# Kernel tuning notes

Hardware: AMD Instinct MI355X
Metric: run time of the kernel (lower is better)

Reference implementation:

```python
import jax, jax.numpy as jnp
import numpy as np

B, N = 32, 512
NFEAT, NHID, NCLASS, NHEADS = 128, 64, 128, 8
WORK_D, SUB_D = 32, 32
H1, H2, OUT_D = 256, 256, 512
ALPHA = 0.2
NEG = -9e15


def setup_inputs() -> dict:
    key = jax.random.key(0)
    ks = jax.random.split(key, 16)
    return {
        "graph_inf": jax.random.normal(ks[0], (B, N, NFEAT), jnp.float32),
        "graph_matrix": jax.random.randint(ks[1], (B, N, N), 0, 2, jnp.int32),
        "masks": jnp.ones((B, N), jnp.float32),
        "node_order": jax.random.randint(ks[2], (B,), 0, N, jnp.int64),
        "work": jax.random.normal(ks[3], (B, WORK_D), jnp.float32),
        "subtask": jax.random.normal(ks[4], (B, SUB_D), jnp.float32),
        # GAT head params
        "W_heads": jax.random.normal(ks[5], (NHEADS, NFEAT, NHID), jnp.float32) * 0.1,
        "a_heads": jax.random.normal(ks[6], (NHEADS, 2 * NHID), jnp.float32) * 0.1,
        "W_out": jax.random.normal(ks[7], (NHID * NHEADS, NCLASS), jnp.float32) * 0.05,
        "a_out": jax.random.normal(ks[8], (2 * NCLASS,), jnp.float32) * 0.1,
        # MLP encoder params
        "fc1_w": jax.random.normal(ks[9], (NCLASS + WORK_D + SUB_D, H1), jnp.float32) * 0.07,
        "fc1_b": jnp.zeros((H1,), jnp.float32),
        "fc2_w": jax.random.normal(ks[10], (H1, H2), jnp.float32) * 0.06,
        "fc2_b": jnp.zeros((H2,), jnp.float32),
        "fc3_w": jax.random.normal(ks[11], (H2, OUT_D), jnp.float32) * 0.06,
        "fc3_b": jnp.zeros((OUT_D,), jnp.float32),
    }


def _gat_layer(Wh, a1, a2, adj, masks):
    # Wh: [B,N,F]; additive GAT score e_ij = leakyrelu(a1.Wh_i + a2.Wh_j)
    s1 = Wh @ a1  # [B,N]
    s2 = Wh @ a2  # [B,N]
    e = jax.nn.leaky_relu(s1[:, :, None] + s2[:, None, :], ALPHA)  # [B,N,N]
    att = jax.nn.softmax(jnp.where(adj > 0, e, NEG), axis=2)
    h_prime = jnp.einsum('bnm,bmf->bnf', att, Wh)
    return h_prime * masks[:, :, None]


def reference(graph_inf, graph_matrix, masks, node_order, work, subtask,
              W_heads, a_heads, W_out, a_out,
              fc1_w, fc1_b, fc2_w, fc2_b, fc3_w, fc3_b):
    adj = graph_matrix
    # multi-head GAT layer (concat=True -> ELU)
    def head(Wk, ak):
        Wh = jnp.einsum('bnf,fo->bno', graph_inf, Wk)
        return jax.nn.elu(_gat_layer(Wh, ak[:NHID], ak[NHID:], adj, masks))
    xh = jax.vmap(head)(W_heads, a_heads)  # [H,B,N,NHID]
    x = jnp.transpose(xh, (1, 2, 0, 3)).reshape(B, N, NHEADS * NHID)
    # output GAT layer (concat=False)
    Wh = jnp.einsum('bnf,fo->bno', x, W_out)
    x = _gat_layer(Wh, a_out[:NCLASS], a_out[NCLASS:], adj, masks)
    x = x * masks[:, :, None]
    # select subtask node per batch element
    selected = x[jnp.arange(B), node_order]  # [B,NCLASS]
    inf = jnp.concatenate([selected, work, subtask], axis=1)
    h = jax.nn.relu(inf @ fc1_w + fc1_b)
    h = jax.nn.relu(h @ fc2_w + fc2_b)
    out = h @ fc3_w + fc3_b
    return jax.nn.softmax(out, axis=-1)
```

## Files before the change

### kernel.cpp

```cpp
#include <hip/hip_runtime.h>

typedef unsigned short u16;
typedef unsigned int u32;
typedef unsigned long long u64;

typedef __bf16 bf16x8 __attribute__((ext_vector_type(8)));
typedef float f32x4 __attribute__((ext_vector_type(4)));

#define LOG2E 1.44269504088896340736f

__device__ __forceinline__ float b2f(u16 u) {
    u32 x = ((u32)u) << 16;
    return __builtin_bit_cast(float, x);
}
__device__ __forceinline__ u16 f2b(float f) {
    u32 u = __builtin_bit_cast(u32, f);
    u32 r = (u + 0x7fffu + ((u >> 16) & 1u)) >> 16;
    return (u16)r;
}
__device__ __forceinline__ float ld(const void* p, int i, bool bf) {
    return bf ? b2f(((const u16*)p)[i]) : ((const float*)p)[i];
}
__device__ __forceinline__ bool detect_bf16(const void* masks) {
    return ((const u16*)masks)[0] != 0;
}
__device__ __forceinline__ f32x4 mfma16(bf16x8 a, bf16x8 b, f32x4 c) {
    return __builtin_amdgcn_mfma_f32_16x16x32_bf16(a, b, c, 0, 0, 0);
}

__device__ __attribute__((aligned(256))) u32  g_adjm[16384 * 16];
__device__ __attribute__((aligned(256))) u16  g_BT1[512 * 128];
__device__ __attribute__((aligned(256))) u16  g_BT2[128 * 512];
__device__ __attribute__((aligned(256))) u16  g_Xc[32 * 512 * 128];
__device__ __attribute__((aligned(256))) u16  g_xb[16384 * 512];
__device__ __attribute__((aligned(256))) u16  g_Wh2[16384 * 128];
__device__ __attribute__((aligned(256))) float g_s1b[16384];
__device__ __attribute__((aligned(256))) float g_s2b[16384];
__device__ __attribute__((aligned(256))) u16  g_fc1T[256 * 192];
__device__ __attribute__((aligned(256))) u16  g_fc2T[256 * 256];
__device__ __attribute__((aligned(256))) u16  g_fc3T[512 * 256];
__device__ __attribute__((aligned(256))) u16  g_Ahi[32 * 192];
__device__ __attribute__((aligned(256))) u16  g_Alo[32 * 192];
__device__ __attribute__((aligned(256))) u16  g_H1hi[32 * 256];
__device__ __attribute__((aligned(256))) u16  g_H1lo[32 * 256];
__device__ __attribute__((aligned(256))) u16  g_H2hi[32 * 256];
__device__ __attribute__((aligned(256))) u16  g_H2lo[32 * 256];
__device__ __attribute__((aligned(256))) float g_logits[32 * 512];

__global__ __launch_bounds__(256) void prep_kernel(
    const int* __restrict__ adj, const void* __restrict__ Whd,
    const void* __restrict__ Wo, const void* __restrict__ Xin,
    const void* __restrict__ fc1w, const void* __restrict__ fc2w,
    const void* __restrict__ fc3w, const void* __restrict__ masks)
{
    const bool bf = detect_bf16(masks);
    const int blk = blockIdx.x;
    const int tid = threadIdx.x;
    if (blk < 1024) {
        int id = blk * 256 + tid;
        int row = id >> 4, w = id & 15;
        const int4* p = (const int4*)(adj + row * 512 + w * 32);
        int4 v[8];
        #pragma unroll
        for (int s = 0; s < 8; ++s) v[s] = p[s];
        u32 word = 0;
        #pragma unroll
        for (int s = 0; s < 8; ++s) {
            u32 nib = (v[s].x > 0 ? 1u : 0u) | (v[s].y > 0 ? 2u : 0u) |
                      (v[s].z > 0 ? 4u : 0u) | (v[s].w > 0 ? 8u : 0u);
            word |= nib << (4 * s);
        }
        g_adjm[id] = word;
    } else if (blk < 1028) {
        int base = (blk - 1024) * 16384;
        for (int e = base + tid; e < base + 16384; e += 256) {
            int n = e >> 7, k = e & 127;
            g_BT1[e] = f2b(ld(Whd, (n >> 6) * 8192 + k * 64 + (n & 63), bf));
        }
    } else if (blk < 1032) {
        int base = (blk - 1028) * 16384;
        for (int e = base + tid; e < base + 16384; e += 256) {
            int n = e >> 9, k = e & 511;
            g_BT2[e] = f2b(ld(Wo, k * 128 + n, bf));
        }
    } else if (blk < 1288) {
        if (!bf) {
            int base = (blk - 1032) * 8192;
            for (int e = base + tid; e < base + 8192; e += 256)
                g_Xc[e] = f2b(((const float*)Xin)[e]);
        }
    } else if (blk < 1294) {
        int base = (blk - 1288) * 8192;
        for (int e = base + tid; e < base + 8192; e += 256) {
            int n = e / 192, k = e - n * 192;
            g_fc1T[e] = f2b(ld(fc1w, k * 256 + n, bf));
        }
    } else if (blk < 1302) {
        int base = (blk - 1294) * 8192;
        for (int e = base + tid; e < base + 8192; e += 256) {
            int n = e >> 8, k = e & 255;
            g_fc2T[e] = f2b(ld(fc2w, k * 256 + n, bf));
        }
    } else {
        int base = (blk - 1302) * 8192;
        for (int e = base + tid; e < base + 8192; e += 256) {
            int n = e >> 8, k = e & 255;
            g_fc3T[e] = f2b(ld(fc3w, k * 512 + n, bf));
        }
    }
}

__global__ __launch_bounds__(1024, 1) void gat1_kernel(
    const void* __restrict__ Xin, const void* __restrict__ a_heads,
    const void* __restrict__ masks)
{
    __shared__ __attribute__((aligned(16))) u16 WhL[64 * 520];
    __shared__ __attribute__((aligned(16))) u16 As[64 * 136];
    __shared__ __attribute__((aligned(16))) u16 XcL[128 * 136];
    __shared__ float s1p[4][512];
    __shared__ float s2p[4][512];
    __shared__ float E2s[512];
    __shared__ float E2ps[512];

    const bool bf = detect_bf16(masks);
    const int tid = threadIdx.x;
    const int w = tid >> 6, lane = tid & 63;
    const int c = lane & 15, q = lane >> 4;
    const int b = blockIdx.x & 31;
    const int h = blockIdx.x >> 5;

    const u16* Bsrc = bf ? (const u16*)Xin : g_Xc;

    {
        int r = tid >> 4, seg = (tid & 15) * 8;
        *(uint4*)&As[r * 136 + seg] = *(const uint4*)(g_BT1 + (h * 64 + r) * 128 + seg);
    }

    const int wm = w & 3, wn = w >> 2;
    float a1v[4], a2v[4];
    #pragma unroll
    for (int i = 0; i < 4; ++i) {
        int o = wm * 16 + q * 4 + i;
        a1v[i] = ld(a_heads, h * 128 + o, bf);
        a2v[i] = ld(a_heads, h * 128 + 64 + o, bf);
    }

    const int pr = tid >> 3, pseg = (tid & 7) * 16;
    uint4 xr0, xr1;
    {
        const u16* src = Bsrc + (b * 512 + pr) * 128 + pseg;
        xr0 = *(const uint4*)src;
        xr1 = *(const uint4*)(src + 8);
    }

    for (int chunk = 0; chunk < 4; ++chunk) {
        __syncthreads();
        *(uint4*)&XcL[pr * 136 + pseg] = xr0;
        *(uint4*)&XcL[pr * 136 + pseg + 8] = xr1;
        if (chunk < 3) {
            const u16* src = Bsrc + (b * 512 + (chunk + 1) * 128 + pr) * 128 + pseg;
            xr0 = *(const uint4*)src;
            xr1 = *(const uint4*)(src + 8);
        }
        __syncthreads();
        f32x4 cacc[2] = {};
        #pragma unroll
        for (int kt = 0; kt < 4; ++kt) {
            bf16x8 af = *(const bf16x8*)&As[(wm * 16 + c) * 136 + kt * 32 + q * 8];
            #pragma unroll
            for (int nt = 0; nt < 2; ++nt) {
                bf16x8 bv = *(const bf16x8*)&XcL[(wn * 32 + nt * 16 + c) * 136 + kt * 32 + q * 8];
                cacc[nt] = mfma16(af, bv, cacc[nt]);
            }
        }
        #pragma unroll
        for (int nt = 0; nt < 2; ++nt) {
            const int ncol = chunk * 128 + wn * 32 + nt * 16 + c;
            float p1 = 0.f, p2 = 0.f;
            #pragma unroll
            for (int i = 0; i < 4; ++i) {
                float v = cacc[nt][i];
                WhL[(wm * 16 + q * 4 + i) * 520 + ncol] = f2b(v);
                p1 += v * a1v[i];
                p2 += v * a2v[i];
            }
            p1 += __shfl_xor(p1, 16); p1 += __shfl_xor(p1, 32);
            p2 += __shfl_xor(p2, 16); p2 += __shfl_xor(p2, 32);
            if (lane < 16) {
                int n = chunk * 128 + wn * 32 + nt * 16 + lane;
                s1p[wm][n] = p1;
// ... 74 lines not shown
        #pragma unroll
        for (int i = 0; i < 4; ++i) {
            float lr = __shfl(acc1[g][i], (lane & 48));
            float invr = (lr == 0.f) ? (1.f / 512.f) : (1.f / lr);
            const int row = R + q * 4 + i;
            float mk = ld(masks, b * 512 + row, bf);
            #pragma unroll
            for (int nt = 0; nt < 4; ++nt) {
                float v = acc[g][nt][i] * invr * mk;
                float o = v > 0.f ? v : (__expf(v) - 1.f);
                g_xb[(b * 512 + row) * 512 + h * 64 + nt * 16 + c] = f2b(o);
            }
        }
    }
}

__global__ __launch_bounds__(256, 2) void gemm2_kernel(
    const void* __restrict__ a_out, const void* __restrict__ masks)
{
    __shared__ __attribute__((aligned(16))) u16 Asl[64 * 72];
    __shared__ __attribute__((aligned(16))) u16 Bsl[128 * 72];
    const int tid = threadIdx.x;
    const int w = tid >> 6, lane = tid & 63;
    const int c = lane & 15, q = lane >> 4;
    const int tm = blockIdx.x * 64;
    const int rowA = tid >> 2, shA = (tid & 3) * 16;
    const int rowB = tid >> 1, shB = (tid & 1) * 32;
    f32x4 acc[8] = {};
    for (int kc = 0; kc < 512; kc += 64) {
        __syncthreads();
        const u16* Ag = g_xb + (tm + rowA) * 512 + kc + shA;
        *(uint4*)&Asl[rowA * 72 + shA] = *(const uint4*)Ag;
        *(uint4*)&Asl[rowA * 72 + shA + 8] = *(const uint4*)(Ag + 8);
        const u16* Bg = g_BT2 + rowB * 512 + kc + shB;
        #pragma unroll
        for (int s = 0; s < 4; ++s)
            *(uint4*)&Bsl[rowB * 72 + shB + 8 * s] = *(const uint4*)(Bg + 8 * s);
        __syncthreads();
        #pragma unroll
        for (int kt = 0; kt < 2; ++kt) {
            bf16x8 av = *(const bf16x8*)&Asl[(w * 16 + c) * 72 + kt * 32 + q * 8];
            #pragma unroll
            for (int ct = 0; ct < 8; ++ct) {
                bf16x8 bv = *(const bf16x8*)&Bsl[(ct * 16 + c) * 72 + kt * 32 + q * 8];
                acc[ct] = mfma16(av, bv, acc[ct]);
            }
        }
    }
    const bool bf = detect_bf16(masks);
    float a1v[8], a2v[8];
    #pragma unroll
    for (int ct = 0; ct < 8; ++ct) {
        a1v[ct] = ld(a_out, ct * 16 + c, bf);
        a2v[ct] = ld(a_out, 128 + ct * 16 + c, bf);
    }
    #pragma unroll
    for (int i = 0; i < 4; ++i) {
        float p1 = 0.f, p2 = 0.f;
        #pragma unroll
        for (int ct = 0; ct < 8; ++ct) {
            p1 += acc[ct][i] * a1v[ct];
            p2 += acc[ct][i] * a2v[ct];
        }
        #pragma unroll
        for (int off = 1; off < 16; off <<= 1) {
            p1 += __shfl_xor(p1, off);
            p2 += __shfl_xor(p2, off);
        }
        if (c == 0) {
            int m = tm + w * 16 + q * 4 + i;
            g_s1b[m] = p1 * LOG2E;
            g_s2b[m] = p2 * LOG2E;
        }
    }
    #pragma unroll
    for (int ct = 0; ct < 8; ++ct)
        #pragma unroll
        for (int i = 0; i < 4; ++i) {
            int m = tm + w * 16 + q * 4 + i;
            g_Wh2[m * 128 + ct * 16 + c] = f2b(acc[ct][i]);
        }
}

__global__ __launch_bounds__(256) void fin_att(
    const void* __restrict__ masks, const int* __restrict__ node_order,
    const void* __restrict__ workv, const void* __restrict__ subtaskv)
{
    __shared__ float att[512];
    __shared__ float parts[16][128];
    __shared__ float redl[4];

    const bool bf = detect_bf16(masks);
    const int b = blockIdx.x, t = threadIdx.x;
    const int lane = t & 63, wv = t >> 6;
    const int istar = node_order[b];

    const float s1v = g_s1b[b * 512 + istar];
    const u32* arow = g_adjm + (b * 512 + istar) * 16;
    float ssum = 0.f;
    #pragma unroll
    for (int rep = 0; rep < 2; ++rep) {
        int j = t + rep * 256;
        float e = s1v + g_s2b[b * 512 + j];
        e = fmaxf(e, 0.2f * e);
        float ex = ((arow[j >> 5] >> (j & 31)) & 1u) ? exp2f(e) : 0.f;
        att[j] = ex;
        ssum += ex;
    }
    for (int off = 1; off < 64; off <<= 1) ssum += __shfl_xor(ssum, off);
    if (lane == 0) redl[wv] = ssum;
    __syncthreads();
    float tot = redl[0] + redl[1] + redl[2] + redl[3];
    bool uni = (tot == 0.f);
    float inv = uni ? (1.f / 512.f) : (1.f / tot);

    const int og = t & 15, jg = t >> 4;
    float acc[8] = {};
    const u16* base = g_Wh2 + (b * 512 + jg * 32) * 128 + og * 8;
    #pragma unroll 8
    for (int j0 = 0; j0 < 32; ++j0) {
        float wgt = uni ? 1.f : att[jg * 32 + j0];
        union { u16 u[8]; uint4 v; } z;
        z.v = *(const uint4*)(base + j0 * 128);
        #pragma unroll
        for (int i = 0; i < 8; ++i) acc[i] += wgt * b2f(z.u[i]);
    }
    #pragma unroll
    for (int i = 0; i < 8; ++i) parts[jg][og * 8 + i] = acc[i];
    __syncthreads();
    float mk = ld(masks, b * 512 + istar, bf);
    if (t < 128) {
        float s = 0.f;
        #pragma unroll
        for (int jj = 0; jj < 16; ++jj) s += parts[jj][t];
        s *= inv * mk * mk;
        u16 hi = f2b(s);
        g_Ahi[b * 192 + t] = hi;
        g_Alo[b * 192 + t] = f2b(s - b2f(hi));
    } else if (t < 160) {
        g_Ahi[b * 192 + t] = bf ? ((const u16*)workv)[b * 32 + t - 128]
                                : f2b(((const float*)workv)[b * 32 + t - 128]);
        g_Alo[b * 192 + t] = 0;
    } else if (t < 192) {
        g_Ahi[b * 192 + t] = bf ? ((const u16*)subtaskv)[b * 32 + t - 160]
                                : f2b(((const float*)subtaskv)[b * 32 + t - 160]);
        g_Alo[b * 192 + t] = 0;
    }
}

template<int K, int NOUT, bool RELU>
__device__ __forceinline__ void mlp_body(
    const u16* __restrict__ Ahi, const u16* __restrict__ Alo,
    const u16* __restrict__ WT, const void* __restrict__ bias,
    u16* __restrict__ Ohi, u16* __restrict__ Olo, float* __restrict__ Of,
    const void* __restrict__ masks)
{
    const bool bf = detect_bf16(masks);
    const int t = threadIdx.x, w = t >> 6, lane = t & 63;
    const int c = lane & 15, q = lane >> 4;
    const int col = blockIdx.x * 64 + w * 16 + c;

    const u16* wp  = WT + col * K + q * 8;
    const u16* ahp = Ahi + c * K + q * 8;
    const u16* alp = Alo + c * K + q * 8;

    f32x4 acc0 = {}, acc1 = {};
    #pragma unroll
    for (int kt = 0; kt < K / 32; ++kt) {
        bf16x8 bw  = *(const bf16x8*)(wp + kt * 32);
        bf16x8 ah0 = *(const bf16x8*)(ahp + kt * 32);
        bf16x8 al0 = *(const bf16x8*)(alp + kt * 32);
        bf16x8 ah1 = *(const bf16x8*)(ahp + 16 * K + kt * 32);
        bf16x8 al1 = *(const bf16x8*)(alp + 16 * K + kt * 32);
        acc0 = mfma16(ah0, bw, acc0);
        acc0 = mfma16(al0, bw, acc0);
        acc1 = mfma16(ah1, bw, acc1);
        acc1 = mfma16(al1, bw, acc1);
    }
    float bs = ld(bias, col, bf);
    #pragma unroll
    for (int mt = 0; mt < 2; ++mt) {
        f32x4 a = mt ? acc1 : acc0;
        #pragma unroll
        for (int i = 0; i < 4; ++i) {
            int m = mt * 16 + q * 4 + i;
            float v = a[i] + bs;
            if (RELU) {
                v = fmaxf(v, 0.f);
                u16 hi = f2b(v);
                Ohi[m * NOUT + col] = hi;
                Olo[m * NOUT + col] = f2b(v - b2f(hi));
            } else {
                Of[m * NOUT + col] = v;
            }
        }
    }
}

__global__ __launch_bounds__(256) void mlp1_kernel(const void* bias, const void* masks) {
    mlp_body<192, 256, true>(g_Ahi, g_Alo, g_fc1T, bias, g_H1hi, g_H1lo, nullptr, masks);
}
__global__ __launch_bounds__(256) void mlp2_kernel(const void* bias, const void* masks) {
    mlp_body<256, 256, true>(g_H1hi, g_H1lo, g_fc2T, bias, g_H2hi, g_H2lo, nullptr, masks);
}
__global__ __launch_bounds__(256) void mlp3_kernel(const void* bias, const void* masks) {
    mlp_body<256, 512, false>(g_H2hi, g_H2lo, g_fc3T, bias, nullptr, nullptr, g_logits, masks);
}

__global__ __launch_bounds__(64) void softmax_kernel(
    const void* __restrict__ masks, void* __restrict__ out)
{
    const bool bf = detect_bf16(masks);
    const int row = blockIdx.x, lane = threadIdx.x;
    const float* lp = g_logits + row * 512 + lane * 8;
    float v[8];
    *(float4*)&v[0] = *(const float4*)lp;
    *(float4*)&v[4] = *(const float4*)(lp + 4);
    float mx = v[0];
    #pragma unroll
    for (int i = 1; i < 8; ++i) mx = fmaxf(mx, v[i]);
    for (int off = 1; off < 64; off <<= 1) mx = fmaxf(mx, __shfl_xor(mx, off));
    float e[8];
    float s = 0.f;
    #pragma unroll
    for (int i = 0; i < 8; ++i) { e[i] = __expf(v[i] - mx); s += e[i]; }
    for (int off = 1; off < 64; off <<= 1) s += __shfl_xor(s, off);
    float inv = 1.f / s;
    if (bf) {
        u16* o = (u16*)out + row * 512 + lane * 8;
        #pragma unroll
        for (int i = 0; i < 8; ++i) o[i] = f2b(e[i] * inv);
    } else {
        float* o = (float*)out + row * 512 + lane * 8;
        #pragma unroll
        for (int i = 0; i < 8; ++i) o[i] = e[i] * inv;
    }
}

extern "C" void kernel_launch(void* const* d_in, const int* in_sizes, int n_in,
                              void* d_out, int out_size, void* d_ws, size_t ws_size,
                              hipStream_t stream)
{
    const void* graph_inf    = d_in[0];
    const int*  graph_matrix = (const int*)d_in[1];
    const void* masks        = d_in[2];
    const int*  node_order   = (const int*)d_in[3];
    const void* work         = d_in[4];
    const void* subtask      = d_in[5];
    const void* W_heads      = d_in[6];
    const void* a_heads      = d_in[7];
    const void* W_out        = d_in[8];
    const void* a_out        = d_in[9];
    const void* fc1w         = d_in[10];
    const void* fc1b         = d_in[11];
    const void* fc2w         = d_in[12];
    const void* fc2b         = d_in[13];
    const void* fc3w         = d_in[14];
    const void* fc3b         = d_in[15];

    prep_kernel<<<dim3(1318), dim3(256), 0, stream>>>(graph_matrix, W_heads, W_out, graph_inf,
                                                      fc1w, fc2w, fc3w, masks);
    gat1_kernel<<<dim3(256), dim3(1024), 0, stream>>>(graph_inf, a_heads, masks);
    gemm2_kernel<<<dim3(256), dim3(256), 0, stream>>>(a_out, masks);
    fin_att<<<dim3(32), dim3(256), 0, stream>>>(masks, node_order, work, subtask);
    mlp1_kernel<<<dim3(4), dim3(256), 0, stream>>>(fc1b, masks);
    mlp2_kernel<<<dim3(4), dim3(256), 0, stream>>>(fc2b, masks);
    mlp3_kernel<<<dim3(8), dim3(256), 0, stream>>>(fc3b, masks);
    softmax_kernel<<<dim3(32), dim3(64), 0, stream>>>(masks, d_out);
}
```

Baseline: 184.8 us.

## Fuse attention readout, MLP and softmax into a single tail kernel

Replaces the final attention row kernel, three MFMA MLP kernels and the softmax kernel with one per-batch kernel that keeps the intermediate activations in shared memory and uses scalar FMAs. The MLP weights are read directly from the inputs, so the transposes in the prep kernel are removed. This cuts four launches and the global round trips between stages. In exchange, each of the 32 blocks streams all MLP weights itself, and the matmuls no longer use matrix cores.

```diff
diff --git a/kernel.cpp b/kernel.cpp
--- a/kernel.cpp
+++ b/kernel.cpp
@@ -20,6 +20,10 @@
 }
 __device__ __forceinline__ float ld(const void* p, int i, bool bf) {
     return bf ? b2f(((const u16*)p)[i]) : ((const float*)p)[i];
+}
+template<bool BF>
+__device__ __forceinline__ float ldt(const void* p, int i) {
+    return BF ? b2f(((const u16*)p)[i]) : ((const float*)p)[i];
 }
 __device__ __forceinline__ bool detect_bf16(const void* masks) {
     return ((const u16*)masks)[0] != 0;
@@ -36,22 +40,11 @@
 __device__ __attribute__((aligned(256))) u16  g_Wh2[16384 * 128];
 __device__ __attribute__((aligned(256))) float g_s1b[16384];
 __device__ __attribute__((aligned(256))) float g_s2b[16384];
-__device__ __attribute__((aligned(256))) u16  g_fc1T[256 * 192];
-__device__ __attribute__((aligned(256))) u16  g_fc2T[256 * 256];
-__device__ __attribute__((aligned(256))) u16  g_fc3T[512 * 256];
-__device__ __attribute__((aligned(256))) u16  g_Ahi[32 * 192];
-__device__ __attribute__((aligned(256))) u16  g_Alo[32 * 192];
-__device__ __attribute__((aligned(256))) u16  g_H1hi[32 * 256];
-__device__ __attribute__((aligned(256))) u16  g_H1lo[32 * 256];
-__device__ __attribute__((aligned(256))) u16  g_H2hi[32 * 256];
-__device__ __attribute__((aligned(256))) u16  g_H2lo[32 * 256];
-__device__ __attribute__((aligned(256))) float g_logits[32 * 512];
 
 __global__ __launch_bounds__(256) void prep_kernel(
     const int* __restrict__ adj, const void* __restrict__ Whd,
     const void* __restrict__ Wo, const void* __restrict__ Xin,
-    const void* __restrict__ fc1w, const void* __restrict__ fc2w,
-    const void* __restrict__ fc3w, const void* __restrict__ masks)
+    const void* __restrict__ masks)
 {
     const bool bf = detect_bf16(masks);
     const int blk = blockIdx.x;
@@ -83,29 +76,11 @@
             int n = e >> 9, k = e & 511;
             g_BT2[e] = f2b(ld(Wo, k * 128 + n, bf));
         }
-    } else if (blk < 1288) {
+    } else {
         if (!bf) {
             int base = (blk - 1032) * 8192;
             for (int e = base + tid; e < base + 8192; e += 256)
                 g_Xc[e] = f2b(((const float*)Xin)[e]);
-        }
-    } else if (blk < 1294) {
-        int base = (blk - 1288) * 8192;
-        for (int e = base + tid; e < base + 8192; e += 256) {
-            int n = e / 192, k = e - n * 192;
-            g_fc1T[e] = f2b(ld(fc1w, k * 256 + n, bf));
-        }
-    } else if (blk < 1302) {
-        int base = (blk - 1294) * 8192;
-        for (int e = base + tid; e < base + 8192; e += 256) {
-            int n = e >> 8, k = e & 255;
-            g_fc2T[e] = f2b(ld(fc2w, k * 256 + n, bf));
-        }
-    } else {
-        int base = (blk - 1302) * 8192;
-        for (int e = base + tid; e < base + 8192; e += 256) {
-            int n = e >> 8, k = e & 255;
-            g_fc3T[e] = f2b(ld(fc3w, k * 512 + n, bf));
         }
     }
 }
@@ -346,15 +321,17 @@
         }
 }
 
-__global__ __launch_bounds__(256) void fin_att(
+template<bool BF>
+__device__ __forceinline__ void tail_body(
     const void* __restrict__ masks, const int* __restrict__ node_order,
-    const void* __restrict__ workv, const void* __restrict__ subtaskv)
+    const void* __restrict__ workv, const void* __restrict__ subtaskv,
+    const void* __restrict__ fc1w, const void* __restrict__ fc1b,
+    const void* __restrict__ fc2w, const void* __restrict__ fc2b,
+    const void* __restrict__ fc3w, const void* __restrict__ fc3b,
+    void* __restrict__ out,
+    float* att, float (*parts)[128], float* redl, float* red2,
+    float* inf_s, float* h1s, float* h2s)
 {
-    __shared__ float att[512];
-    __shared__ float parts[16][128];
-    __shared__ float redl[4];
-
-    const bool bf = detect_bf16(masks);
     const int b = blockIdx.x, t = threadIdx.x;
     const int lane = t & 63, wv = t >> 6;
     const int istar = node_order[b];
@@ -392,113 +369,108 @@
     #pragma unroll
     for (int i = 0; i < 8; ++i) parts[jg][og * 8 + i] = acc[i];
     __syncthreads();
-    float mk = ld(masks, b * 512 + istar, bf);
+
+    float mk = ldt<BF>(masks, b * 512 + istar);
     if (t < 128) {
         float s = 0.f;
         #pragma unroll
         for (int jj = 0; jj < 16; ++jj) s += parts[jj][t];
-        s *= inv * mk * mk;
-        u16 hi = f2b(s);
-        g_Ahi[b * 192 + t] = hi;
-        g_Alo[b * 192 + t] = f2b(s - b2f(hi));
+        inf_s[t] = s * inv * mk * mk;
     } else if (t < 160) {
-        g_Ahi[b * 192 + t] = bf ? ((const u16*)workv)[b * 32 + t - 128]
-                                : f2b(((const float*)workv)[b * 32 + t - 128]);
-        g_Alo[b * 192 + t] = 0;
+        inf_s[t] = ldt<BF>(workv, b * 32 + t - 128);
     } else if (t < 192) {
-        g_Ahi[b * 192 + t] = bf ? ((const u16*)subtaskv)[b * 32 + t - 160]
-                                : f2b(((const float*)subtaskv)[b * 32 + t - 160]);
-        g_Alo[b * 192 + t] = 0;
-    }
-}
-
-template<int K, int NOUT, bool RELU>
-__device__ __forceinline__ void mlp_body(
-    const u16* __restrict__ Ahi, const u16* __restrict__ Alo,
-    const u16* __restrict__ WT, const void* __restrict__ bias,
-    u16* __restrict__ Ohi, u16* __restrict__ Olo, float* __restrict__ Of,
-    const void* __restrict__ masks)
+        inf_s[t] = ldt<BF>(subtaskv, b * 32 + t - 160);
+    }
+    __syncthreads();
+
+    {
+        float a0 = 0.f, a1 = 0.f, a2 = 0.f, a3 = 0.f;
+        #pragma unroll 4
+        for (int k = 0; k < 192; k += 4) {
+            a0 += inf_s[k]     * ldt<BF>(fc1w, k * 256 + t);
+            a1 += inf_s[k + 1] * ldt<BF>(fc1w, (k + 1) * 256 + t);
+            a2 += inf_s[k + 2] * ldt<BF>(fc1w, (k + 2) * 256 + t);
+            a3 += inf_s[k + 3] * ldt<BF>(fc1w, (k + 3) * 256 + t);
+        }
+        float v = (a0 + a1) + (a2 + a3) + ldt<BF>(fc1b, t);
+        h1s[t] = fmaxf(v, 0.f);
+    }
+    __syncthreads();
+
+    {
+        float a0 = 0.f, a1 = 0.f, a2 = 0.f, a3 = 0.f;
+        #pragma unroll 4
+        for (int k = 0; k < 256; k += 4) {
+            a0 += h1s[k]     * ldt<BF>(fc2w, k * 256 + t);
+            a1 += h1s[k + 1] * ldt<BF>(fc2w, (k + 1) * 256 + t);
+            a2 += h1s[k + 2] * ldt<BF>(fc2w, (k + 2) * 256 + t);
+            a3 += h1s[k + 3] * ldt<BF>(fc2w, (k + 3) * 256 + t);
+        }
+        float v = (a0 + a1) + (a2 + a3) + ldt<BF>(fc2b, t);
+        h2s[t] = fmaxf(v, 0.f);
+    }
+    __syncthreads();
+
+    float lg0, lg1;
+    {
+        float b0 = 0.f, b1 = 0.f, c0 = 0.f, c1 = 0.f;
+        #pragma unroll 4
+        for (int k = 0; k < 256; k += 2) {
+            float hv0 = h2s[k], hv1 = h2s[k + 1];
+            b0 += hv0 * ldt<BF>(fc3w, k * 512 + t);
+            c0 += hv0 * ldt<BF>(fc3w, k * 512 + 256 + t);
+            b1 += hv1 * ldt<BF>(fc3w, (k + 1) * 512 + t);
+            c1 += hv1 * ldt<BF>(fc3w, (k + 1) * 512 + 256 + t);
+        }
+        lg0 = b0 + b1 + ldt<BF>(fc3b, t);
+        lg1 = c0 + c1 + ldt<BF>(fc3b, 256 + t);
+    }
+
+    float mx = fmaxf(lg0, lg1);
+    #pragma unroll
+    for (int off = 1; off < 64; off <<= 1) mx = fmaxf(mx, __shfl_xor(mx, off));
+    if (lane == 0) redl[wv] = mx;
+    __syncthreads();
+    mx = fmaxf(fmaxf(redl[0], redl[1]), fmaxf(redl[2], redl[3]));
+    float e0 = __expf(lg0 - mx), e1 = __expf(lg1 - mx);
+    float s = e0 + e1;
+    #pragma unroll
+    for (int off = 1; off < 64; off <<= 1) s += __shfl_xor(s, off);
+    if (lane == 0) red2[wv] = s;
+    __syncthreads();
+    float invs = 1.f / (red2[0] + red2[1] + red2[2] + red2[3]);
+    if (BF) {
+        u16* o = (u16*)out + b * 512;
+        o[t]       = f2b(e0 * invs);
+        o[256 + t] = f2b(e1 * invs);
+    } else {
+        float* o = (float*)out + b * 512;
+        o[t]       = e0 * invs;
+        o[256 + t] = e1 * invs;
+    }
+}
+
+__global__ __launch_bounds__(256) void tail_kernel(
+    const void* __restrict__ masks, const int* __restrict__ node_order,
+    const void* __restrict__ workv, const void* __restrict__ subtaskv,
+    const void* __restrict__ fc1w, const void* __restrict__ fc1b,
+    const void* __restrict__ fc2w, const void* __restrict__ fc2b,
+    const void* __restrict__ fc3w, const void* __restrict__ fc3b,
+    void* __restrict__ out)
 {
-    const bool bf = detect_bf16(masks);
-    const int t = threadIdx.x, w = t >> 6, lane = t & 63;
-    const int c = lane & 15, q = lane >> 4;
-    const int col = blockIdx.x * 64 + w * 16 + c;
-
-    const u16* wp  = WT + col * K + q * 8;
-    const u16* ahp = Ahi + c * K + q * 8;
-    const u16* alp = Alo + c * K + q * 8;
-
-    f32x4 acc0 = {}, acc1 = {};
-    #pragma unroll
-    for (int kt = 0; kt < K / 32; ++kt) {
-        bf16x8 bw  = *(const bf16x8*)(wp + kt * 32);
-        bf16x8 ah0 = *(const bf16x8*)(ahp + kt * 32);
-        bf16x8 al0 = *(const bf16x8*)(alp + kt * 32);
-        bf16x8 ah1 = *(const bf16x8*)(ahp + 16 * K + kt * 32);
-        bf16x8 al1 = *(const bf16x8*)(alp + 16 * K + kt * 32);
-        acc0 = mfma16(ah0, bw, acc0);
-        acc0 = mfma16(al0, bw, acc0);
-        acc1 = mfma16(ah1, bw, acc1);
-        acc1 = mfma16(al1, bw, acc1);
-    }
-    float bs = ld(bias, col, bf);
-    #pragma unroll
-    for (int mt = 0; mt < 2; ++mt) {
-        f32x4 a = mt ? acc1 : acc0;
-        #pragma unroll
-        for (int i = 0; i < 4; ++i) {
-            int m = mt * 16 + q * 4 + i;
-            float v = a[i] + bs;
-            if (RELU) {
-                v = fmaxf(v, 0.f);
-                u16 hi = f2b(v);
-                Ohi[m * NOUT + col] = hi;
-                Olo[m * NOUT + col] = f2b(v - b2f(hi));
-            } else {
-                Of[m * NOUT + col] = v;
-            }
-        }
-    }
-}
-
-__global__ __launch_bounds__(256) void mlp1_kernel(const void* bias, const void* masks) {
-    mlp_body<192, 256, true>(g_Ahi, g_Alo, g_fc1T, bias, g_H1hi, g_H1lo, nullptr, masks);
-}
-__global__ __launch_bounds__(256) void mlp2_kernel(const void* bias, const void* masks) {
-    mlp_body<256, 256, true>(g_H1hi, g_H1lo, g_fc2T, bias, g_H2hi, g_H2lo, nullptr, masks);
-}
-__global__ __launch_bounds__(256) void mlp3_kernel(const void* bias, const void* masks) {
-    mlp_body<256, 512, false>(g_H2hi, g_H2lo, g_fc3T, bias, nullptr, nullptr, g_logits, masks);
-}
-
-__global__ __launch_bounds__(64) void softmax_kernel(
-    const void* __restrict__ masks, void* __restrict__ out)
-{
-    const bool bf = detect_bf16(masks);
-    const int row = blockIdx.x, lane = threadIdx.x;
-    const float* lp = g_logits + row * 512 + lane * 8;
-    float v[8];
-    *(float4*)&v[0] = *(const float4*)lp;
-    *(float4*)&v[4] = *(const float4*)(lp + 4);
-    float mx = v[0];
-    #pragma unroll
-    for (int i = 1; i < 8; ++i) mx = fmaxf(mx, v[i]);
-    for (int off = 1; off < 64; off <<= 1) mx = fmaxf(mx, __shfl_xor(mx, off));
-    float e[8];
-    float s = 0.f;
-    #pragma unroll
-    for (int i = 0; i < 8; ++i) { e[i] = __expf(v[i] - mx); s += e[i]; }
-    for (int off = 1; off < 64; off <<= 1) s += __shfl_xor(s, off);
-    float inv = 1.f / s;
-    if (bf) {
-        u16* o = (u16*)out + row * 512 + lane * 8;
-        #pragma unroll
-        for (int i = 0; i < 8; ++i) o[i] = f2b(e[i] * inv);
-    } else {
-        float* o = (float*)out + row * 512 + lane * 8;
-        #pragma unroll
-        for (int i = 0; i < 8; ++i) o[i] = e[i] * inv;
-    }
+    __shared__ float att[512];
+    __shared__ float parts[16][128];
+    __shared__ float redl[4];
+    __shared__ float red2[4];
+    __shared__ float inf_s[192];
+    __shared__ float h1s[256];
+    __shared__ float h2s[256];
+    if (detect_bf16(masks))
+        tail_body<true>(masks, node_order, workv, subtaskv, fc1w, fc1b, fc2w, fc2b,
+                        fc3w, fc3b, out, att, parts, redl, red2, inf_s, h1s, h2s);
+    else
+        tail_body<false>(masks, node_order, workv, subtaskv, fc1w, fc1b, fc2w, fc2b,
+                         fc3w, fc3b, out, att, parts, redl, red2, inf_s, h1s, h2s);
 }
 
 extern "C" void kernel_launch(void* const* d_in, const int* in_sizes, int n_in,
@@ -522,13 +494,11 @@
     const void* fc3w         = d_in[14];
     const void* fc3b         = d_in[15];
 
-    prep_kernel<<<dim3(1318), dim3(256), 0, stream>>>(graph_matrix, W_heads, W_out, graph_inf,
-                                                      fc1w, fc2w, fc3w, masks);
+    prep_kernel<<<dim3(1288), dim3(256), 0, stream>>>(graph_matrix, W_heads, W_out,
+                                                      graph_inf, masks);
     gat1_kernel<<<dim3(256), dim3(1024), 0, stream>>>(graph_inf, a_heads, masks);
     gemm2_kernel<<<dim3(256), dim3(256), 0, stream>>>(a_out, masks);
-    fin_att<<<dim3(32), dim3(256), 0, stream>>>(masks, node_order, work, subtask);
-    mlp1_kernel<<<dim3(4), dim3(256), 0, stream>>>(fc1b, masks);
-    mlp2_kernel<<<dim3(4), dim3(256), 0, stream>>>(fc2b, masks);
-    mlp3_kernel<<<dim3(8), dim3(256), 0, stream>>>(fc3b, masks);
-    softmax_kernel<<<dim3(32), dim3(64), 0, stream>>>(masks, d_out);
-}
+    tail_kernel<<<dim3(32), dim3(256), 0, stream>>>(masks, node_order, work, subtask,
+                                                    fc1w, fc1b, fc2w, fc2b, fc3w, fc3b,
+                                                    d_out);
+}
```

Result: slower. 193.0 us (+4.4%).

## Fuse three MLP layers and softmax into one single-block kernel

Applied to the files above, without the earlier changes.

Replaces the four small launches (mlp1, mlp2, mlp3, softmax) with one 1024-thread block that keeps the hidden activations in LDS and does the softmax with cross-wave reductions. This removes three kernel launches and the global round trips for the intermediate activations and logits. The cost is that all MLP work now runs on a single CU instead of several, so the weight loads and MFMAs are serialized on one compute unit.

```diff
diff --git a/kernel.cpp b/kernel.cpp
--- a/kernel.cpp
+++ b/kernel.cpp
@@ -41,11 +41,6 @@
 __device__ __attribute__((aligned(256))) u16  g_fc3T[512 * 256];
 __device__ __attribute__((aligned(256))) u16  g_Ahi[32 * 192];
 __device__ __attribute__((aligned(256))) u16  g_Alo[32 * 192];
-__device__ __attribute__((aligned(256))) u16  g_H1hi[32 * 256];
-__device__ __attribute__((aligned(256))) u16  g_H1lo[32 * 256];
-__device__ __attribute__((aligned(256))) u16  g_H2hi[32 * 256];
-__device__ __attribute__((aligned(256))) u16  g_H2lo[32 * 256];
-__device__ __attribute__((aligned(256))) float g_logits[32 * 512];
 
 __global__ __launch_bounds__(256) void prep_kernel(
     const int* __restrict__ adj, const void* __restrict__ Whd,
@@ -412,93 +407,179 @@
     }
 }
 
-template<int K, int NOUT, bool RELU>
-__device__ __forceinline__ void mlp_body(
-    const u16* __restrict__ Ahi, const u16* __restrict__ Alo,
-    const u16* __restrict__ WT, const void* __restrict__ bias,
-    u16* __restrict__ Ohi, u16* __restrict__ Olo, float* __restrict__ Of,
-    const void* __restrict__ masks)
+__global__ __launch_bounds__(1024) void mlp_fused(
+    const void* __restrict__ fc1b, const void* __restrict__ fc2b,
+    const void* __restrict__ fc3b, const void* __restrict__ masks,
+    void* __restrict__ out)
 {
+    __shared__ __attribute__((aligned(16))) u16 H1hi[32 * 264];
+    __shared__ __attribute__((aligned(16))) u16 H1lo[32 * 264];
+    __shared__ __attribute__((aligned(16))) u16 H2hi[32 * 264];
+    __shared__ __attribute__((aligned(16))) u16 H2lo[32 * 264];
+    __shared__ float pred[32][16];
+    __shared__ float rred[32];
+
     const bool bf = detect_bf16(masks);
     const int t = threadIdx.x, w = t >> 6, lane = t & 63;
     const int c = lane & 15, q = lane >> 4;
-    const int col = blockIdx.x * 64 + w * 16 + c;
-
-    const u16* wp  = WT + col * K + q * 8;
-    const u16* ahp = Ahi + c * K + q * 8;
-    const u16* alp = Alo + c * K + q * 8;
-
-    f32x4 acc0 = {}, acc1 = {};
-    #pragma unroll
-    for (int kt = 0; kt < K / 32; ++kt) {
-        bf16x8 bw  = *(const bf16x8*)(wp + kt * 32);
-        bf16x8 ah0 = *(const bf16x8*)(ahp + kt * 32);
-        bf16x8 al0 = *(const bf16x8*)(alp + kt * 32);
-        bf16x8 ah1 = *(const bf16x8*)(ahp + 16 * K + kt * 32);
-        bf16x8 al1 = *(const bf16x8*)(alp + 16 * K + kt * 32);
-        acc0 = mfma16(ah0, bw, acc0);
-        acc0 = mfma16(al0, bw, acc0);
-        acc1 = mfma16(ah1, bw, acc1);
-        acc1 = mfma16(al1, bw, acc1);
-    }
-    float bs = ld(bias, col, bf);
-    #pragma unroll
-    for (int mt = 0; mt < 2; ++mt) {
-        f32x4 a = mt ? acc1 : acc0;
+
+    {
+        const int col = w * 16 + c;
+        const u16* wp  = g_fc1T + col * 192 + q * 8;
+        const u16* ahp = g_Ahi + c * 192 + q * 8;
+        const u16* alp = g_Alo + c * 192 + q * 8;
+        f32x4 acc0 = {}, acc1 = {};
+        #pragma unroll
+        for (int kt = 0; kt < 6; ++kt) {
+            bf16x8 bw  = *(const bf16x8*)(wp + kt * 32);
+            bf16x8 ah0 = *(const bf16x8*)(ahp + kt * 32);
+            bf16x8 al0 = *(const bf16x8*)(alp + kt * 32);
+            bf16x8 ah1 = *(const bf16x8*)(ahp + 16 * 192 + kt * 32);
+            bf16x8 al1 = *(const bf16x8*)(alp + 16 * 192 + kt * 32);
+            acc0 = mfma16(ah0, bw, acc0);
+            acc0 = mfma16(al0, bw, acc0);
+            acc1 = mfma16(ah1, bw, acc1);
+            acc1 = mfma16(al1, bw, acc1);
+        }
+        float bs = ld(fc1b, col, bf);
+        #pragma unroll
+        for (int mt = 0; mt < 2; ++mt) {
+            f32x4 a = mt ? acc1 : acc0;
+            #pragma unroll
+            for (int i = 0; i < 4; ++i) {
+                int m = mt * 16 + q * 4 + i;
+                float v = fmaxf(a[i] + bs, 0.f);
+                u16 hi = f2b(v);
+                H1hi[m * 264 + col] = hi;
+                H1lo[m * 264 + col] = f2b(v - b2f(hi));
+            }
+        }
+    }
+    __syncthreads();
+
+    {
+        const int col = w * 16 + c;
+        const u16* wp  = g_fc2T + col * 256 + q * 8;
+        const u16* ahp = H1hi + c * 264 + q * 8;
+        const u16* alp = H1lo + c * 264 + q * 8;
+        f32x4 acc0 = {}, acc1 = {};
+        #pragma unroll
+        for (int kt = 0; kt < 8; ++kt) {
+            bf16x8 bw  = *(const bf16x8*)(wp + kt * 32);
+            bf16x8 ah0 = *(const bf16x8*)(ahp + kt * 32);
+            bf16x8 al0 = *(const bf16x8*)(alp + kt * 32);
+            bf16x8 ah1 = *(const bf16x8*)(ahp + 16 * 264 + kt * 32);
+            bf16x8 al1 = *(const bf16x8*)(alp + 16 * 264 + kt * 32);
+            acc0 = mfma16(ah0, bw, acc0);
+            acc0 = mfma16(al0, bw, acc0);
+            acc1 = mfma16(ah1, bw, acc1);
+            acc1 = mfma16(al1, bw, acc1);
+        }
+        float bs = ld(fc2b, col, bf);
+        #pragma unroll
+        for (int mt = 0; mt < 2; ++mt) {
+            f32x4 a = mt ? acc1 : acc0;
+            #pragma unroll
+            for (int i = 0; i < 4; ++i) {
+                int m = mt * 16 + q * 4 + i;
+                float v = fmaxf(a[i] + bs, 0.f);
+                u16 hi = f2b(v);
+                H2hi[m * 264 + col] = hi;
+                H2lo[m * 264 + col] = f2b(v - b2f(hi));
+            }
+        }
+    }
+    __syncthreads();
+
+    float lg[2][2][4];
+    {
+        const u16* ahp = H2hi + c * 264 + q * 8;
+        const u16* alp = H2lo + c * 264 + q * 8;
+        f32x4 acc[2][2] = {};
+        #pragma unroll
+        for (int kt = 0; kt < 8; ++kt) {
+            bf16x8 ah0 = *(const bf16x8*)(ahp + kt * 32);
+            bf16x8 al0 = *(const bf16x8*)(alp + kt * 32);
+            bf16x8 ah1 = *(const bf16x8*)(ahp + 16 * 264 + kt * 32);
+            bf16x8 al1 = *(const bf16x8*)(alp + 16 * 264 + kt * 32);
+            #pragma unroll
+            for (int ct = 0; ct < 2; ++ct) {
+                const int col = w * 32 + ct * 16 + c;
+                bf16x8 bw = *(const bf16x8*)(g_fc3T + col * 256 + kt * 32 + q * 8);
+                acc[ct][0] = mfma16(ah0, bw, acc[ct][0]);
+                acc[ct][0] = mfma16(al0, bw, acc[ct][0]);
+                acc[ct][1] = mfma16(ah1, bw, acc[ct][1]);
+                acc[ct][1] = mfma16(al1, bw, acc[ct][1]);
+            }
+        }
+        #pragma unroll
+        for (int ct = 0; ct < 2; ++ct) {
+            float bs = ld(fc3b, w * 32 + ct * 16 + c, bf);
+            #pragma unroll
+            for (int mt = 0; mt < 2; ++mt)
+                #pragma unroll
+                for (int i = 0; i < 4; ++i)
+                    lg[ct][mt][i] = acc[ct][mt][i] + bs;
+        }
+    }
+
+    #pragma unroll
+    for (int mt = 0; mt < 2; ++mt)
+        #pragma unroll
+        for (int i = 0; i < 4; ++i) {
+            float m = fmaxf(lg[0][mt][i], lg[1][mt][i]);
+            m = fmaxf(m, __shfl_xor(m, 1));
+            m = fmaxf(m, __shfl_xor(m, 2));
+            m = fmaxf(m, __shfl_xor(m, 4));
+            m = fmaxf(m, __shfl_xor(m, 8));
+            if (c == 0) pred[mt * 16 + q * 4 + i][w] = m;
+        }
+    __syncthreads();
+    if (t < 32) {
+        float m = pred[t][0];
+        #pragma unroll
+        for (int j = 1; j < 16; ++j) m = fmaxf(m, pred[t][j]);
+        rred[t] = m;
+    }
+    __syncthreads();
+    #pragma unroll
+    for (int mt = 0; mt < 2; ++mt)
+        #pragma unroll
+        for (int i = 0; i < 4; ++i) {
+            float mx = rred[mt * 16 + q * 4 + i];
+            float e0 = __expf(lg[0][mt][i] - mx);
+            float e1 = __expf(lg[1][mt][i] - mx);
+            lg[0][mt][i] = e0;
+            lg[1][mt][i] = e1;
+            float s = e0 + e1;
+            s += __shfl_xor(s, 1);
+            s += __shfl_xor(s, 2);
+            s += __shfl_xor(s, 4);
+            s += __shfl_xor(s, 8);
+            if (c == 0) pred[mt * 16 + q * 4 + i][w] = s;
+        }
+    __syncthreads();
+    if (t < 32) {
+        float s = 0.f;
+        #pragma unroll
+        for (int j = 0; j < 16; ++j) s += pred[t][j];
+        rred[t] = 1.f / s;
+    }
+    __syncthreads();
+    #pragma unroll
+    for (int mt = 0; mt < 2; ++mt)
         #pragma unroll
         for (int i = 0; i < 4; ++i) {
             int m = mt * 16 + q * 4 + i;
-            float v = a[i] + bs;
-            if (RELU) {
-                v = fmaxf(v, 0.f);
-                u16 hi = f2b(v);
-                Ohi[m * NOUT + col] = hi;
-                Olo[m * NOUT + col] = f2b(v - b2f(hi));
-            } else {
-                Of[m * NOUT + col] = v;
-            }
-        }
-    }
-}
-
-__global__ __launch_bounds__(256) void mlp1_kernel(const void* bias, const void* masks) {
-    mlp_body<192, 256, true>(g_Ahi, g_Alo, g_fc1T, bias, g_H1hi, g_H1lo, nullptr, masks);
-}
-__global__ __launch_bounds__(256) void mlp2_kernel(const void* bias, const void* masks) {
-    mlp_body<256, 256, true>(g_H1hi, g_H1lo, g_fc2T, bias, g_H2hi, g_H2lo, nullptr, masks);
-}
-__global__ __launch_bounds__(256) void mlp3_kernel(const void* bias, const void* masks) {
-    mlp_body<256, 512, false>(g_H2hi, g_H2lo, g_fc3T, bias, nullptr, nullptr, g_logits, masks);
-}
-
-__global__ __launch_bounds__(64) void softmax_kernel(
-    const void* __restrict__ masks, void* __restrict__ out)
-{
-    const bool bf = detect_bf16(masks);
-    const int row = blockIdx.x, lane = threadIdx.x;
-    const float* lp = g_logits + row * 512 + lane * 8;
-    float v[8];
-    *(float4*)&v[0] = *(const float4*)lp;
-    *(float4*)&v[4] = *(const float4*)(lp + 4);
-    float mx = v[0];
-    #pragma unroll
-    for (int i = 1; i < 8; ++i) mx = fmaxf(mx, v[i]);
-    for (int off = 1; off < 64; off <<= 1) mx = fmaxf(mx, __shfl_xor(mx, off));
-    float e[8];
-    float s = 0.f;
-    #pragma unroll
-    for (int i = 0; i < 8; ++i) { e[i] = __expf(v[i] - mx); s += e[i]; }
-    for (int off = 1; off < 64; off <<= 1) s += __shfl_xor(s, off);
-    float inv = 1.f / s;
-    if (bf) {
-        u16* o = (u16*)out + row * 512 + lane * 8;
-        #pragma unroll
-        for (int i = 0; i < 8; ++i) o[i] = f2b(e[i] * inv);
-    } else {
-        float* o = (float*)out + row * 512 + lane * 8;
-        #pragma unroll
-        for (int i = 0; i < 8; ++i) o[i] = e[i] * inv;
-    }
+            float inv = rred[m];
+            #pragma unroll
+            for (int ct = 0; ct < 2; ++ct) {
+                int col = w * 32 + ct * 16 + c;
+                float v = lg[ct][mt][i] * inv;
+                if (bf) ((u16*)out)[m * 512 + col] = f2b(v);
+                else    ((float*)out)[m * 512 + col] = v;
+            }
+        }
 }
 
 extern "C" void kernel_launch(void* const* d_in, const int* in_sizes, int n_in,
@@ -527,8 +608,5 @@
     gat1_kernel<<<dim3(256), dim3(1024), 0, stream>>>(graph_inf, a_heads, masks);
     gemm2_kernel<<<dim3(256), dim3(256), 0, stream>>>(a_out, masks);
     fin_att<<<dim3(32), dim3(256), 0, stream>>>(masks, node_order, work, subtask);
-    mlp1_kernel<<<dim3(4), dim3(256), 0, stream>>>(fc1b, masks);
-    mlp2_kernel<<<dim3(4), dim3(256), 0, stream>>>(fc2b, masks);
-    mlp3_kernel<<<dim3(8), dim3(256), 0, stream>>>(fc3b, masks);
-    softmax_kernel<<<dim3(32), dim3(64), 0, stream>>>(masks, d_out);
-}
+    mlp_fused<<<dim3(1), dim3(1024), 0, stream>>>(fc1b, fc2b, fc3b, masks, d_out);
+}
```

Measured after the change: 196.4 us. 6.3% more time.

## Fuse tail stages into one persistent kernel with software grid barriers

Applied to the files above, without the earlier changes.

Replaces the five small tail kernels (attention readout, three MLP layers, softmax) with one 32-block kernel that separates the stages with an atomic-counter grid barrier. The goal is to remove four kernel launch gaps on tiny workloads. The MLP stages are split across fewer blocks and waves (half the waves sit idle), and the spin barrier depends on all 32 blocks being resident at once.

```diff
diff --git a/kernel.cpp b/kernel.cpp
--- a/kernel.cpp
+++ b/kernel.cpp
@@ -46,6 +46,27 @@
 __device__ __attribute__((aligned(256))) u16  g_H2hi[32 * 256];
 __device__ __attribute__((aligned(256))) u16  g_H2lo[32 * 256];
 __device__ __attribute__((aligned(256))) float g_logits[32 * 512];
+
+__device__ u32 g_bar_cnt = 0;
+__device__ u32 g_bar_gen = 0;
+
+__device__ __forceinline__ void grid_bar() {
+    __syncthreads();
+    if (threadIdx.x == 0) {
+        __threadfence();
+        u32 my = __hip_atomic_load(&g_bar_gen, __ATOMIC_RELAXED, __HIP_MEMORY_SCOPE_AGENT);
+        u32 old = __hip_atomic_fetch_add(&g_bar_cnt, 1u, __ATOMIC_ACQ_REL, __HIP_MEMORY_SCOPE_AGENT);
+        if (old == 31u) {
+            __hip_atomic_store(&g_bar_cnt, 0u, __ATOMIC_RELAXED, __HIP_MEMORY_SCOPE_AGENT);
+            __hip_atomic_fetch_add(&g_bar_gen, 1u, __ATOMIC_RELEASE, __HIP_MEMORY_SCOPE_AGENT);
+        } else {
+            while (__hip_atomic_load(&g_bar_gen, __ATOMIC_ACQUIRE, __HIP_MEMORY_SCOPE_AGENT) == my)
+                __builtin_amdgcn_s_sleep(8);
+        }
+        __threadfence();
+    }
+    __syncthreads();
+}
 
 __global__ __launch_bounds__(256) void prep_kernel(
     const int* __restrict__ adj, const void* __restrict__ Whd,
@@ -346,158 +367,151 @@
         }
 }
 
-__global__ __launch_bounds__(256) void fin_att(
+template<int K, int NOUT, bool RELU>
+__device__ __forceinline__ void fc_stage(
+    const u16* __restrict__ Ahi, const u16* __restrict__ Alo,
+    const u16* __restrict__ WT, const void* __restrict__ bias,
+    u16* __restrict__ Ohi, u16* __restrict__ Olo, float* __restrict__ Of,
+    bool bf, int colbase)
+{
+    const int t = threadIdx.x, w = t >> 6, lane = t & 63;
+    const int c = lane & 15, q = lane >> 4;
+    if (w >= 2) return;
+    const int col = colbase + c;
+    const u16* wp  = WT + col * K + q * 8;
+    const u16* ahp = Ahi + w * 16 * K + c * K + q * 8;
+    const u16* alp = Alo + w * 16 * K + c * K + q * 8;
+    f32x4 acc = {};
+    #pragma unroll
+    for (int kt = 0; kt < K / 32; ++kt) {
+        bf16x8 bw = *(const bf16x8*)(wp + kt * 32);
+        acc = mfma16(*(const bf16x8*)(ahp + kt * 32), bw, acc);
+        acc = mfma16(*(const bf16x8*)(alp + kt * 32), bw, acc);
+    }
+    float bs = ld(bias, col, bf);
+    #pragma unroll
+    for (int i = 0; i < 4; ++i) {
+        int m = w * 16 + q * 4 + i;
+        float v = acc[i] + bs;
+        if (RELU) {
+            v = fmaxf(v, 0.f);
+            u16 hi = f2b(v);
+            Ohi[m * NOUT + col] = hi;
+            Olo[m * NOUT + col] = f2b(v - b2f(hi));
+        } else {
+            Of[m * NOUT + col] = v;
+        }
+    }
+}
+
+__global__ __launch_bounds__(256, 1) void tailz_kernel(
     const void* __restrict__ masks, const int* __restrict__ node_order,
-    const void* __restrict__ workv, const void* __restrict__ subtaskv)
+    const void* __restrict__ workv, const void* __restrict__ subtaskv,
+    const void* __restrict__ fc1b, const void* __restrict__ fc2b,
+    const void* __restrict__ fc3b, void* __restrict__ out)
 {
     __shared__ float att[512];
     __shared__ float parts[16][128];
     __shared__ float redl[4];
+    __shared__ float red2[4];
 
     const bool bf = detect_bf16(masks);
     const int b = blockIdx.x, t = threadIdx.x;
     const int lane = t & 63, wv = t >> 6;
-    const int istar = node_order[b];
-
-    const float s1v = g_s1b[b * 512 + istar];
-    const u32* arow = g_adjm + (b * 512 + istar) * 16;
-    float ssum = 0.f;
-    #pragma unroll
-    for (int rep = 0; rep < 2; ++rep) {
-        int j = t + rep * 256;
-        float e = s1v + g_s2b[b * 512 + j];
-        e = fmaxf(e, 0.2f * e);
-        float ex = ((arow[j >> 5] >> (j & 31)) & 1u) ? exp2f(e) : 0.f;
-        att[j] = ex;
-        ssum += ex;
-    }
-    for (int off = 1; off < 64; off <<= 1) ssum += __shfl_xor(ssum, off);
-    if (lane == 0) redl[wv] = ssum;
-    __syncthreads();
-    float tot = redl[0] + redl[1] + redl[2] + redl[3];
-    bool uni = (tot == 0.f);
-    float inv = uni ? (1.f / 512.f) : (1.f / tot);
-
-    const int og = t & 15, jg = t >> 4;
-    float acc[8] = {};
-    const u16* base = g_Wh2 + (b * 512 + jg * 32) * 128 + og * 8;
-    #pragma unroll 8
-    for (int j0 = 0; j0 < 32; ++j0) {
-        float wgt = uni ? 1.f : att[jg * 32 + j0];
-        union { u16 u[8]; uint4 v; } z;
-        z.v = *(const uint4*)(base + j0 * 128);
-        #pragma unroll
-        for (int i = 0; i < 8; ++i) acc[i] += wgt * b2f(z.u[i]);
-    }
-    #pragma unroll
-    for (int i = 0; i < 8; ++i) parts[jg][og * 8 + i] = acc[i];
-    __syncthreads();
-    float mk = ld(masks, b * 512 + istar, bf);
-    if (t < 128) {
-        float s = 0.f;
-        #pragma unroll
-        for (int jj = 0; jj < 16; ++jj) s += parts[jj][t];
-        s *= inv * mk * mk;
-        u16 hi = f2b(s);
-        g_Ahi[b * 192 + t] = hi;
-        g_Alo[b * 192 + t] = f2b(s - b2f(hi));
-    } else if (t < 160) {
-        g_Ahi[b * 192 + t] = bf ? ((const u16*)workv)[b * 32 + t - 128]
-                                : f2b(((const float*)workv)[b * 32 + t - 128]);
-        g_Alo[b * 192 + t] = 0;
-    } else if (t < 192) {
-        g_Ahi[b * 192 + t] = bf ? ((const u16*)subtaskv)[b * 32 + t - 160]
-                                : f2b(((const float*)subtaskv)[b * 32 + t - 160]);
-        g_Alo[b * 192 + t] = 0;
-    }
-}
-
-template<int K, int NOUT, bool RELU>
-__device__ __forceinline__ void mlp_body(
-    const u16* __restrict__ Ahi, const u16* __restrict__ Alo,
-    const u16* __restrict__ WT, const void* __restrict__ bias,
-    u16* __restrict__ Ohi, u16* __restrict__ Olo, float* __restrict__ Of,
-    const void* __restrict__ masks)
-{
-    const bool bf = detect_bf16(masks);
-    const int t = threadIdx.x, w = t >> 6, lane = t & 63;
-    const int c = lane & 15, q = lane >> 4;
-    const int col = blockIdx.x * 64 + w * 16 + c;
-
-    const u16* wp  = WT + col * K + q * 8;
-    const u16* ahp = Ahi + c * K + q * 8;
-    const u16* alp = Alo + c * K + q * 8;
-
-    f32x4 acc0 = {}, acc1 = {};
-    #pragma unroll
-    for (int kt = 0; kt < K / 32; ++kt) {
-        bf16x8 bw  = *(const bf16x8*)(wp + kt * 32);
-        bf16x8 ah0 = *(const bf16x8*)(ahp + kt * 32);
-        bf16x8 al0 = *(const bf16x8*)(alp + kt * 32);
-        bf16x8 ah1 = *(const bf16x8*)(ahp + 16 * K + kt * 32);
-        bf16x8 al1 = *(const bf16x8*)(alp + 16 * K + kt * 32);
-        acc0 = mfma16(ah0, bw, acc0);
-        acc0 = mfma16(al0, bw, acc0);
-        acc1 = mfma16(ah1, bw, acc1);
-        acc1 = mfma16(al1, bw, acc1);
-    }
-    float bs = ld(bias, col, bf);
-    #pragma unroll
-    for (int mt = 0; mt < 2; ++mt) {
-        f32x4 a = mt ? acc1 : acc0;
-        #pragma unroll
-        for (int i = 0; i < 4; ++i) {
-            int m = mt * 16 + q * 4 + i;
-            float v = a[i] + bs;
-            if (RELU) {
-                v = fmaxf(v, 0.f);
-                u16 hi = f2b(v);
-                Ohi[m * NOUT + col] = hi;
-                Olo[m * NOUT + col] = f2b(v - b2f(hi));
-            } else {
-                Of[m * NOUT + col] = v;
-            }
-        }
-    }
-}
-
-__global__ __launch_bounds__(256) void mlp1_kernel(const void* bias, const void* masks) {
-    mlp_body<192, 256, true>(g_Ahi, g_Alo, g_fc1T, bias, g_H1hi, g_H1lo, nullptr, masks);
-}
-__global__ __launch_bounds__(256) void mlp2_kernel(const void* bias, const void* masks) {
-    mlp_body<256, 256, true>(g_H1hi, g_H1lo, g_fc2T, bias, g_H2hi, g_H2lo, nullptr, masks);
-}
-__global__ __launch_bounds__(256) void mlp3_kernel(const void* bias, const void* masks) {
-    mlp_body<256, 512, false>(g_H2hi, g_H2lo, g_fc3T, bias, nullptr, nullptr, g_logits, masks);
-}
-
-__global__ __launch_bounds__(64) void softmax_kernel(
-    const void* __restrict__ masks, void* __restrict__ out)
-{
-    const bool bf = detect_bf16(masks);
-    const int row = blockIdx.x, lane = threadIdx.x;
-    const float* lp = g_logits + row * 512 + lane * 8;
-    float v[8];
-    *(float4*)&v[0] = *(const float4*)lp;
-    *(float4*)&v[4] = *(const float4*)(lp + 4);
-    float mx = v[0];
-    #pragma unroll
-    for (int i = 1; i < 8; ++i) mx = fmaxf(mx, v[i]);
-    for (int off = 1; off < 64; off <<= 1) mx = fmaxf(mx, __shfl_xor(mx, off));
-    float e[8];
-    float s = 0.f;
-    #pragma unroll
-    for (int i = 0; i < 8; ++i) { e[i] = __expf(v[i] - mx); s += e[i]; }
-    for (int off = 1; off < 64; off <<= 1) s += __shfl_xor(s, off);
-    float inv = 1.f / s;
-    if (bf) {
-        u16* o = (u16*)out + row * 512 + lane * 8;
-        #pragma unroll
-        for (int i = 0; i < 8; ++i) o[i] = f2b(e[i] * inv);
-    } else {
-        float* o = (float*)out + row * 512 + lane * 8;
-        #pragma unroll
-        for (int i = 0; i < 8; ++i) o[i] = e[i] * inv;
+
+    {
+        const int istar = node_order[b];
+        const float s1v = g_s1b[b * 512 + istar];
+        const u32* arow = g_adjm + (b * 512 + istar) * 16;
+        float ssum = 0.f;
+        #pragma unroll
+        for (int rep = 0; rep < 2; ++rep) {
+            int j = t + rep * 256;
+            float e = s1v + g_s2b[b * 512 + j];
+            e = fmaxf(e, 0.2f * e);
+            float ex = ((arow[j >> 5] >> (j & 31)) & 1u) ? exp2f(e) : 0.f;
+            att[j] = ex;
+            ssum += ex;
+        }
+        for (int off = 1; off < 64; off <<= 1) ssum += __shfl_xor(ssum, off);
+        if (lane == 0) redl[wv] = ssum;
+        __syncthreads();
+        float tot = redl[0] + redl[1] + redl[2] + redl[3];
+        bool uni = (tot == 0.f);
+        float inv = uni ? (1.f / 512.f) : (1.f / tot);
+
+        const int og = t & 15, jg = t >> 4;
+        float acc[8] = {};
+        const u16* base = g_Wh2 + (b * 512 + jg * 32) * 128 + og * 8;
+        #pragma unroll 8
+        for (int j0 = 0; j0 < 32; ++j0) {
+            float wgt = uni ? 1.f : att[jg * 32 + j0];
+            union { u16 u[8]; uint4 v; } z;
+            z.v = *(const uint4*)(base + j0 * 128);
+            #pragma unroll
+            for (int i = 0; i < 8; ++i) acc[i] += wgt * b2f(z.u[i]);
+        }
+        #pragma unroll
+        for (int i = 0; i < 8; ++i) parts[jg][og * 8 + i] = acc[i];
+        __syncthreads();
+        float mk = ld(masks, b * 512 + istar, bf);
+        if (t < 128) {
+            float s = 0.f;
+            #pragma unroll
+            for (int jj = 0; jj < 16; ++jj) s += parts[jj][t];
+            s *= inv * mk * mk;
+            u16 hi = f2b(s);
+            g_Ahi[b * 192 + t] = hi;
+            g_Alo[b * 192 + t] = f2b(s - b2f(hi));
+        } else if (t < 160) {
+            g_Ahi[b * 192 + t] = bf ? ((const u16*)workv)[b * 32 + t - 128]
+                                    : f2b(((const float*)workv)[b * 32 + t - 128]);
+            g_Alo[b * 192 + t] = 0;
+        } else if (t < 192) {
+            g_Ahi[b * 192 + t] = bf ? ((const u16*)subtaskv)[b * 32 + t - 160]
+                                    : f2b(((const float*)subtaskv)[b * 32 + t - 160]);
+            g_Alo[b * 192 + t] = 0;
+        }
+    }
+    grid_bar();
+
+    if (b < 16)
+        fc_stage<192, 256, true>(g_Ahi, g_Alo, g_fc1T, fc1b, g_H1hi, g_H1lo,
+                                 nullptr, bf, b * 16);
+    grid_bar();
+
+    if (b < 16)
+        fc_stage<256, 256, true>(g_H1hi, g_H1lo, g_fc2T, fc2b, g_H2hi, g_H2lo,
+                                 nullptr, bf, b * 16);
+    grid_bar();
+
+    fc_stage<256, 512, false>(g_H2hi, g_H2lo, g_fc3T, fc3b, nullptr, nullptr,
+                              g_logits, bf, b * 16);
+    grid_bar();
+
+    {
+        const float* lp = g_logits + b * 512;
+        float lg0 = lp[t], lg1 = lp[t + 256];
+        float mx = fmaxf(lg0, lg1);
+        for (int off = 1; off < 64; off <<= 1) mx = fmaxf(mx, __shfl_xor(mx, off));
+        if (lane == 0) redl[wv] = mx;
+        __syncthreads();
+        mx = fmaxf(fmaxf(redl[0], redl[1]), fmaxf(redl[2], redl[3]));
+        float e0 = __expf(lg0 - mx), e1 = __expf(lg1 - mx);
+        float s = e0 + e1;
+        for (int off = 1; off < 64; off <<= 1) s += __shfl_xor(s, off);
+        if (lane == 0) red2[wv] = s;
+        __syncthreads();
+        float invs = 1.f / (red2[0] + red2[1] + red2[2] + red2[3]);
+        if (bf) {
+            u16* o = (u16*)out + b * 512;
+            o[t]       = f2b(e0 * invs);
+            o[t + 256] = f2b(e1 * invs);
+        } else {
+            float* o = (float*)out + b * 512;
+            o[t]       = e0 * invs;
+            o[t + 256] = e1 * invs;
+        }
     }
 }
 
@@ -526,9 +540,6 @@
                                                       fc1w, fc2w, fc3w, masks);
     gat1_kernel<<<dim3(256), dim3(1024), 0, stream>>>(graph_inf, a_heads, masks);
     gemm2_kernel<<<dim3(256), dim3(256), 0, stream>>>(a_out, masks);
-    fin_att<<<dim3(32), dim3(256), 0, stream>>>(masks, node_order, work, subtask);
-    mlp1_kernel<<<dim3(4), dim3(256), 0, stream>>>(fc1b, masks);
-    mlp2_kernel<<<dim3(4), dim3(256), 0, stream>>>(fc2b, masks);
-    mlp3_kernel<<<dim3(8), dim3(256), 0, stream>>>(fc3b, masks);
-    softmax_kernel<<<dim3(32), dim3(64), 0, stream>>>(masks, d_out);
-}
+    tailz_kernel<<<dim3(32), dim3(256), 0, stream>>>(masks, node_order, work, subtask,
+                                                     fc1b, fc2b, fc3b, d_out);
+}
```

Result: slower. 190.3 us (+2.9%).
